# Kernel optimization log

Hardware: AMD Instinct MI355X
Metric: run time of the kernel (lower is better)

The kernel has to match this reference:

```python
import jax, jax.numpy as jnp
import numpy as np

NUM_HEADS = 12
HEAD_SIZE = 64
HIDDEN = NUM_HEADS * HEAD_SIZE  # 768
SEQ = 4096


def setup_inputs() -> dict:
    key = jax.random.key(0)
    ks = jax.random.split(key, 7)
    s = 0.02
    return {
        "hidden_states": jax.random.normal(ks[0], (1, SEQ, HIDDEN), jnp.float32),
        "attention_mask": jnp.zeros((1, 1, 1, SEQ), jnp.float32),
        "Wq": jax.random.normal(ks[1], (HIDDEN, HIDDEN), jnp.float32) * s,
        "bq": jax.random.normal(ks[2], (HIDDEN,), jnp.float32) * s,
        "Wk": jax.random.normal(ks[3], (HIDDEN, HIDDEN), jnp.float32) * s,
        "bk": jax.random.normal(ks[4], (HIDDEN,), jnp.float32) * s,
        "Wv": jax.random.normal(ks[5], (HIDDEN, HIDDEN), jnp.float32) * s,
        "bv": jax.random.normal(ks[6], (HIDDEN,), jnp.float32) * s,
    }


def _split_heads(x):
    # [B, S, H] -> [B, nh, S, hd]
    B, S, _ = x.shape
    return x.reshape(B, S, NUM_HEADS, HEAD_SIZE).transpose(0, 2, 1, 3)


def reference(hidden_states, attention_mask, Wq, bq, Wk, bk, Wv, bv):
    # torch Linear: y = x @ W.T + b
    q = _split_heads(hidden_states @ Wq.T + bq)  # [B, nh, S, hd]
    k = _split_heads(hidden_states @ Wk.T + bk)
    scores = jnp.einsum("bhqd,bhkd->bhqk", q, k) / jnp.sqrt(
        jnp.asarray(HEAD_SIZE, hidden_states.dtype)
    )
    scores = scores + attention_mask  # broadcast [1,1,1,S]
    probs = jax.nn.softmax(scores, axis=-1)  # [B, nh, S, S]
    # multi_rand_attn_cuda is a Monte-Carlo approximation of the exact
    # aggregation: probs @ (hidden @ Wv.T + bv), per head. The reference
    # computes the exact expected value (deterministic equivalent).
    v = _split_heads(hidden_states @ Wv.T + bv)  # [B, nh, S, hd]
    ctx = jnp.einsum("bhqk,bhkd->bhqd", probs, v)  # [B, nh, S, hd]
    B, _, S, _ = ctx.shape
    ctx = ctx.transpose(0, 2, 1, 3).reshape(B, S, HIDDEN)
    return ctx
```

## Files before the change

kernel.cpp:

```cpp
#include <hip/hip_runtime.h>
#include <hip/hip_bf16.h>

#define SEQ 4096
#define HID 768
#define NHEAD 12
#define HDIM 64
#define KVB 64
#define NT (SEQ / KVB)
#define PBK 64
#define PNT (HID / PBK)

typedef __attribute__((ext_vector_type(8))) short bf16x8;
typedef __attribute__((ext_vector_type(4))) float f32x4;
typedef __attribute__((ext_vector_type(4))) short s16x4;

static __device__ __forceinline__ short f2bf(float f) {
    unsigned u = __builtin_bit_cast(unsigned, f);
    unsigned r = (u + 0x7fffu + ((u >> 16) & 1u)) >> 16;
    return (short)r;
}
static __device__ __forceinline__ float bf2f(unsigned short u) {
    return __builtin_bit_cast(float, (unsigned)u << 16);
}
static __device__ __forceinline__ unsigned cvtpk(float lo, float hi) {
    unsigned r;
    asm("v_cvt_pk_bf16_f32 %0, %1, %2" : "=v"(r) : "v"(lo), "v"(hi));
    return r;
}
static __device__ __forceinline__ float max3f(float a, float b, float c) {
    float r;
    asm("v_max3_f32 %0, %1, %2, %3" : "=v"(r) : "v"(a), "v"(b), "v"(c));
    return r;
}
static __device__ __forceinline__ void glds16(const void* g, void* l) {
    __builtin_amdgcn_global_load_lds(
        (const __attribute__((address_space(1))) unsigned*)g,
        (__attribute__((address_space(3))) unsigned*)l, 16, 0, 0);
}

__global__ __launch_bounds__(256) void cast_bf16_kernel(
    const float* __restrict__ src, short* __restrict__ dst)
{
    const size_t i = (size_t)blockIdx.x * 256 + threadIdx.x;
    const float4* s = reinterpret_cast<const float4*>(src) + i * 2;
    const float4 a = s[0], b = s[1];
    bf16x8 o;
    o[0] = f2bf(a.x); o[1] = f2bf(a.y); o[2] = f2bf(a.z); o[3] = f2bf(a.w);
    o[4] = f2bf(b.x); o[5] = f2bf(b.y); o[6] = f2bf(b.z); o[7] = f2bf(b.w);
    reinterpret_cast<bf16x8*>(dst)[i] = o;
}

__global__ __launch_bounds__(256) void cast_w_kernel(
    const float* __restrict__ Wq, const float* __restrict__ Wk,
    const float* __restrict__ Wv, short* __restrict__ dst)
{
    const int z = blockIdx.y;
    const float* src = (z == 0) ? Wq : ((z == 1) ? Wk : Wv);
    const size_t i = (size_t)blockIdx.x * 256 + threadIdx.x;
    const float4* s = reinterpret_cast<const float4*>(src) + i * 2;
    const float4 a = s[0], b = s[1];
    bf16x8 o;
    o[0] = f2bf(a.x); o[1] = f2bf(a.y); o[2] = f2bf(a.z); o[3] = f2bf(a.w);
    o[4] = f2bf(b.x); o[5] = f2bf(b.y); o[6] = f2bf(b.z); o[7] = f2bf(b.w);
    reinterpret_cast<bf16x8*>(dst + (size_t)z * HID * HID)[i] = o;
}

__global__ __launch_bounds__(256) void qkv_proj_kernel(
    const short* __restrict__ hsb, const short* __restrict__ Wb,
    const float* __restrict__ bq, const float* __restrict__ bk,
    const float* __restrict__ bv,
    short* __restrict__ Qb, short* __restrict__ Kb, short* __restrict__ Vt)
{
    __shared__ __align__(16) char lds[65536];
    const int z = blockIdx.z;
    const float* bias = (z == 0) ? bq : ((z == 1) ? bk : bv);

    const int lane = threadIdx.x & 63;
    const int w    = threadIdx.x >> 6;
    const int lr = lane & 15, hi = lane >> 4;
    const int wi = w >> 1, wj = w & 1;

    const short* Ag; const short* Bg; int ar0, br0;
    if (z < 2) { Ag = Wb + (size_t)z * HID * HID; ar0 = blockIdx.x * 128;
                 Bg = hsb;                        br0 = blockIdx.y * 128; }
    else       { Ag = hsb;                        ar0 = blockIdx.y * 128;
                 Bg = Wb + (size_t)2 * HID * HID; br0 = blockIdx.x * 128; }

    const int rsub = lane >> 3;
    const int c16  = (lane & 7) ^ rsub;

    auto stage = [&](int t, int buf) {
        const int k0 = t * PBK;
#pragma unroll
        for (int c = 0; c < 4; ++c) {
            const int ch = w * 4 + c;
            const int row = ch * 8 + rsub;
            glds16(Ag + (size_t)(ar0 + row) * HID + k0 + c16 * 8,
                   lds + buf * 16384 + ch * 1024);
            glds16(Bg + (size_t)(br0 + row) * HID + k0 + c16 * 8,
                   lds + 32768 + buf * 16384 + ch * 1024);
        }
    };

    stage(0, 0);
    f32x4 acc[4][4] = {};

    for (int t = 0; t < PNT; ++t) {
        asm volatile("s_waitcnt vmcnt(0)" ::: "memory");
        __builtin_amdgcn_s_barrier();
        __builtin_amdgcn_sched_barrier(0);
        if (t + 1 < PNT) stage(t + 1, (t + 1) & 1);
        const char* LA = lds + (t & 1) * 16384;
        const char* LB = lds + 32768 + (t & 1) * 16384;
#pragma unroll
        for (int ks = 0; ks < 2; ++ks) {
            bf16x8 af[4], bf_[4];
#pragma unroll
            for (int i = 0; i < 4; ++i) {
                const int rowA = wi * 64 + i * 16 + lr;
                af[i] = *reinterpret_cast<const bf16x8*>(
                    LA + rowA * 128 + (((ks * 4 + hi) ^ (rowA & 7)) << 4));
                const int rowB = wj * 64 + i * 16 + lr;
                bf_[i] = *reinterpret_cast<const bf16x8*>(
                    LB + rowB * 128 + (((ks * 4 + hi) ^ (rowB & 7)) << 4));
            }
            __builtin_amdgcn_s_setprio(1);
#pragma unroll
            for (int ia = 0; ia < 4; ++ia)
#pragma unroll
                for (int ib = 0; ib < 4; ++ib)
                    acc[ia][ib] = __builtin_amdgcn_mfma_f32_16x16x32_bf16(
                        af[ia], bf_[ib], acc[ia][ib], 0, 0, 0);
            __builtin_amdgcn_s_setprio(0);
        }
    }

    const float SCQ = 0.125f * 1.44269504088896340736f;
    if (z < 2) {
        short* outp = (z == 0) ? Qb : Kb;
        const float sc = (z == 0) ? SCQ : 1.0f;
#pragma unroll
        for (int ia = 0; ia < 4; ++ia) {
            const int nb = ar0 + wi * 64 + ia * 16 + hi * 4;
            const float4 b4 = *reinterpret_cast<const float4*>(bias + nb);
#pragma unroll
            for (int ib = 0; ib < 4; ++ib) {
                const int m = br0 + wj * 64 + ib * 16 + lr;
                s16x4 v;
                v[0] = f2bf((acc[ia][ib][0] + b4.x) * sc);
                v[1] = f2bf((acc[ia][ib][1] + b4.y) * sc);
                v[2] = f2bf((acc[ia][ib][2] + b4.z) * sc);
                v[3] = f2bf((acc[ia][ib][3] + b4.w) * sc);
                *reinterpret_cast<s16x4*>(outp + (size_t)m * HID + nb) = v;
            }
        }
    } else {
#pragma unroll
        for (int ib = 0; ib < 4; ++ib) {
            const int n = br0 + wj * 64 + ib * 16 + lr;
            const float bb = bias[n];
#pragma unroll
            for (int ia = 0; ia < 4; ++ia) {
                const int mb = ar0 + wi * 64 + ia * 16 + hi * 4;
                s16x4 v;
                v[0] = f2bf(acc[ia][ib][0] + bb);
                v[1] = f2bf(acc[ia][ib][1] + bb);
                v[2] = f2bf(acc[ia][ib][2] + bb);
                v[3] = f2bf(acc[ia][ib][3] + bb);
                *reinterpret_cast<s16x4*>(Vt + (size_t)n * SEQ + mb) = v;
            }
        }
    }
}

__global__ __launch_bounds__(256, 4) void attn_kernel(
    const short* __restrict__ Qb, const short* __restrict__ Kb,
    const short* __restrict__ Vt, const float* __restrict__ maskp,
    float* __restrict__ out)
{
    __shared__ __align__(16) char lds[40960];
    const int tid  = threadIdx.x;
    const int lane = tid & 63;
    const int w    = tid >> 6;
    const int lr = lane & 15, hi = lane >> 4;
    const int h  = blockIdx.y;
    const int q0 = blockIdx.x * 64 + w * 16;
    const float ML = 1.44269504088896340736f;

    const int srow = lane >> 3;
    auto stage = [&](int t, int buf) {
        const int kt = t * KVB;
#pragma unroll
        for (int j = 0; j < 2; ++j) {
            const int ch  = w * 2 + j;
            const int row = ch * 8 + srow;
            const int c16 = (lane & 7) ^ srow ^ ((ch & 1) << 2);
            glds16(Kb + (size_t)(kt + row) * HID + h * HDIM + c16 * 8,
                   lds + buf * 8192 + ch * 1024);
            glds16(Vt + (size_t)(h * HDIM + row) * SEQ + kt + c16 * 8,
                   lds + 16384 + buf * 8192 + ch * 1024);
        }
    };

    stage(0, 0);

    {
        short* mb = (short*)(lds + 32768);
        const int base = tid * 16;
#pragma unroll
        for (int i = 0; i < 4; ++i) {
            const float4 m4 = *reinterpret_cast<const float4*>(maskp + base + i * 4);
            s16x4 v;
            v[0] = f2bf(m4.x * ML); v[1] = f2bf(m4.y * ML);
            v[2] = f2bf(m4.z * ML); v[3] = f2bf(m4.w * ML);
            *reinterpret_cast<s16x4*>(mb + base + i * 4) = v;
        }
    }

    const short* qp = Qb + (size_t)(q0 + lr) * HID + h * HDIM + hi * 8;
    const bf16x8 qa0 = *reinterpret_cast<const bf16x8*>(qp);
    const bf16x8 qa1 = *reinterpret_cast<const bf16x8*>(qp + 32);

    __syncthreads();

    f32x4 oAcc[4] = {};
    float m_r = -INFINITY, ls = 0.f;
    const short* mlds = (const short*)(lds + 32768);

    const int kbase = ((lr >> 2) * 8) + (lr & 3);
    const int fv    = (lr & 7) ^ ((lr >> 1) & 4);

    for (int t = 0; t < NT; ++t) {
        const int kt = t * KVB;
        asm volatile("s_waitcnt vmcnt(0)" ::: "memory");
        __builtin_amdgcn_s_barrier();
        __builtin_amdgcn_sched_barrier(0);
        if (t + 1 < NT) stage(t + 1, (t + 1) & 1);

        const char* KT = lds + (t & 1) * 8192;
        float s2[4][4];
#pragma unroll
        for (int g = 0; g < 4; ++g) {
            const int mk0 = hi * 8 + (g & 1) * 4 + (g >> 1) * 32;
            const s16x4 mkv = *reinterpret_cast<const s16x4*>(mlds + kt + mk0);
            f32x4 zz;
            zz[0] = bf2f((unsigned short)mkv[0]);
            zz[1] = bf2f((unsigned short)mkv[1]);
            zz[2] = bf2f((unsigned short)mkv[2]);
            zz[3] = bf2f((unsigned short)mkv[3]);
            const int row = kbase + (g & 1) * 4 + (g >> 1) * 32;
            const int fr  = (row & 7) ^ ((row >> 1) & 4);
            const bf16x8 kf0 = *reinterpret_cast<const bf16x8*>(
                KT + row * 128 + ((hi ^ fr) << 4));
            const bf16x8 kf1 = *reinterpret_cast<const bf16x8*>(
                KT + row * 128 + (((4 + hi) ^ fr) << 4));
            __builtin_amdgcn_s_setprio(1);
            zz = __builtin_amdgcn_mfma_f32_16x16x32_bf16(kf0, qa0, zz, 0, 0, 0);
            zz = __builtin_amdgcn_mfma_f32_16x16x32_bf16(kf1, qa1, zz, 0, 0, 0);
            __builtin_amdgcn_s_setprio(0);
            s2[g][0] = zz[0]; s2[g][1] = zz[1]; s2[g][2] = zz[2]; s2[g][3] = zz[3];
        }

        float tmax;
        {
            const float a = max3f(s2[0][0], s2[0][1], s2[0][2]);
            const float b = max3f(s2[0][3], s2[1][0], s2[1][1]);
            const float c = max3f(s2[1][2], s2[1][3], s2[2][0]);
            const float d = max3f(s2[2][1], s2[2][2], s2[2][3]);
            const float e = max3f(s2[3][0], s2[3][1], s2[3][2]);
            tmax = max3f(max3f(a, b, c), max3f(d, e, s2[3][3]),
                         __builtin_bit_cast(float, 0xff800000u));
        }
        tmax = fmaxf(tmax, __shfl_xor(tmax, 16));
        tmax = fmaxf(tmax, __shfl_xor(tmax, 32));

        if (__ballot(tmax > m_r + 8.f)) {
            const float newm = fmaxf(m_r, tmax);
            const float sc = exp2f(fmaxf(m_r - newm, -128.f));
            ls *= sc;
#pragma unroll
            for (int c = 0; c < 4; ++c) oAcc[c] *= sc;
            m_r = newm;
        }

        float e_[4][4];
#pragma unroll
        for (int g = 0; g < 4; ++g) {
#pragma unroll
            for (int r = 0; r < 4; ++r) {
                e_[g][r] = exp2f(s2[g][r] - m_r);
                ls += e_[g][r];
            }
        }
        union { unsigned u[4]; bf16x8 v; } P0, P1;
        P0.u[0] = cvtpk(e_[0][0], e_[0][1]); P0.u[1] = cvtpk(e_[0][2], e_[0][3]);
        P0.u[2] = cvtpk(e_[1][0], e_[1][1]); P0.u[3] = cvtpk(e_[1][2], e_[1][3]);
        P1.u[0] = cvtpk(e_[2][0], e_[2][1]); P1.u[1] = cvtpk(e_[2][2], e_[2][3]);
        P1.u[2] = cvtpk(e_[3][0], e_[3][1]); P1.u[3] = cvtpk(e_[3][2], e_[3][3]);

        const char* VT = lds + 16384 + (t & 1) * 8192;
#pragma unroll
        for (int dg = 0; dg < 4; ++dg) {
            const int rb = (dg * 16 + lr) * 128;
            const bf16x8 v0 = *reinterpret_cast<const bf16x8*>(VT + rb + ((hi ^ fv) << 4));
            const bf16x8 v1 = *reinterpret_cast<const bf16x8*>(VT + rb + (((4 + hi) ^ fv) << 4));
            __builtin_amdgcn_s_setprio(1);
            oAcc[dg] = __builtin_amdgcn_mfma_f32_16x16x32_bf16(v0, P0.v, oAcc[dg], 0, 0, 0);
            oAcc[dg] = __builtin_amdgcn_mfma_f32_16x16x32_bf16(v1, P1.v, oAcc[dg], 0, 0, 0);
            __builtin_amdgcn_s_setprio(0);
        }
    }

    float lt = ls;
    lt += __shfl_xor(lt, 16);
    lt += __shfl_xor(lt, 32);
    const float rl = 1.0f / lt;
    float* ob = out + (size_t)(q0 + lr) * HID + h * HDIM + hi * 4;
#pragma unroll
    for (int dg = 0; dg < 4; ++dg)
        *reinterpret_cast<f32x4*>(ob + dg * 16) = oAcc[dg] * rl;
}

extern "C" void kernel_launch(void* const* d_in, const int* in_sizes, int n_in,
                              void* d_out, int out_size, void* d_ws, size_t ws_size,
                              hipStream_t stream) {
    const float* hs   = (const float*)d_in[0];
    const float* mask = (const float*)d_in[1];
    const float* Wq   = (const float*)d_in[2];
    const float* bq   = (const float*)d_in[3];
    const float* Wk   = (const float*)d_in[4];
    const float* bk   = (const float*)d_in[5];
    const float* Wv   = (const float*)d_in[6];
    const float* bv   = (const float*)d_in[7];

    short* Qb = (short*)d_ws;
    short* Kb = Qb + (size_t)SEQ * HID;
    short* Vt = Kb + (size_t)SEQ * HID;
    float* out = (float*)d_out;

    short* hsb = (short*)d_out;
    short* Wb  = hsb + (size_t)SEQ * HID;

    cast_bf16_kernel<<<dim3(SEQ * HID / 2048), 256, 0, stream>>>(hs, hsb);
    cast_w_kernel<<<dim3(HID * HID / 2048, 3), 256, 0, stream>>>(Wq, Wk, Wv, Wb);

    qkv_proj_kernel<<<dim3(HID / 128, SEQ / 128, 3), 256, 0, stream>>>(
        hsb, Wb, bq, bk, bv, Qb, Kb, Vt);

    attn_kernel<<<dim3(SEQ / KVB, NHEAD), 256, 0, stream>>>(Qb, Kb, Vt, mask, out);
}
```

Before: 151.9 us.

## Split KV tile across wave pairs, each wave handling 32 queries with merge

Each block's four waves are reorganised into two query halves times two key halves. Every wave now processes 32 queries against half of each 64-key tile, so each K and V fragment read from LDS feeds two MFMAs. The two key halves are merged at the end through LDS using max/sum rescaling. The mask is kept as fp32 in LDS and loaded straight in as the MFMA accumulator init instead of being converted from bf16. The cost is more registers and LDS per block, with occupancy lowered to 3, plus an extra merge phase with two block barriers.

```diff
diff --git a/kernel.cpp b/kernel.cpp
--- a/kernel.cpp
+++ b/kernel.cpp
@@ -18,9 +18,6 @@
     unsigned u = __builtin_bit_cast(unsigned, f);
     unsigned r = (u + 0x7fffu + ((u >> 16) & 1u)) >> 16;
     return (short)r;
-}
-static __device__ __forceinline__ float bf2f(unsigned short u) {
-    return __builtin_bit_cast(float, (unsigned)u << 16);
 }
 static __device__ __forceinline__ unsigned cvtpk(float lo, float hi) {
     unsigned r;
@@ -173,18 +170,19 @@
     }
 }
 
-__global__ __launch_bounds__(256, 4) void attn_kernel(
+__global__ __launch_bounds__(256, 3) void attn_kernel(
     const short* __restrict__ Qb, const short* __restrict__ Kb,
     const short* __restrict__ Vt, const float* __restrict__ maskp,
     float* __restrict__ out)
 {
-    __shared__ __align__(16) char lds[40960];
+    __shared__ __align__(16) char lds[49152];
     const int tid  = threadIdx.x;
     const int lane = tid & 63;
     const int w    = tid >> 6;
     const int lr = lane & 15, hi = lane >> 4;
+    const int qh = w >> 1, kh = w & 1;
     const int h  = blockIdx.y;
-    const int q0 = blockIdx.x * 64 + w * 16;
+    const int q0 = blockIdx.x * 64 + qh * 32;
     const float ML = 1.44269504088896340736f;
 
     const int srow = lane >> 3;
@@ -205,120 +203,164 @@
     stage(0, 0);
 
     {
-        short* mb = (short*)(lds + 32768);
+        float* mb = (float*)(lds + 32768);
         const int base = tid * 16;
 #pragma unroll
         for (int i = 0; i < 4; ++i) {
-            const float4 m4 = *reinterpret_cast<const float4*>(maskp + base + i * 4);
-            s16x4 v;
-            v[0] = f2bf(m4.x * ML); v[1] = f2bf(m4.y * ML);
-            v[2] = f2bf(m4.z * ML); v[3] = f2bf(m4.w * ML);
-            *reinterpret_cast<s16x4*>(mb + base + i * 4) = v;
-        }
-    }
-
-    const short* qp = Qb + (size_t)(q0 + lr) * HID + h * HDIM + hi * 8;
-    const bf16x8 qa0 = *reinterpret_cast<const bf16x8*>(qp);
-    const bf16x8 qa1 = *reinterpret_cast<const bf16x8*>(qp + 32);
+            float4 m4 = *reinterpret_cast<const float4*>(maskp + base + i * 4);
+            m4.x *= ML; m4.y *= ML; m4.z *= ML; m4.w *= ML;
+            *reinterpret_cast<float4*>(mb + base + i * 4) = m4;
+        }
+    }
+
+    const short* qbase = Qb + (size_t)(q0 + lr) * HID + h * HDIM + hi * 8;
+    bf16x8 qf[2][2];
+    qf[0][0] = *reinterpret_cast<const bf16x8*>(qbase);
+    qf[0][1] = *reinterpret_cast<const bf16x8*>(qbase + 32);
+    qf[1][0] = *reinterpret_cast<const bf16x8*>(qbase + 16 * HID);
+    qf[1][1] = *reinterpret_cast<const bf16x8*>(qbase + 16 * HID + 32);
 
     __syncthreads();
 
-    f32x4 oAcc[4] = {};
-    float m_r = -INFINITY, ls = 0.f;
-    const short* mlds = (const short*)(lds + 32768);
-
-    const int kbase = ((lr >> 2) * 8) + (lr & 3);
-    const int fv    = (lr & 7) ^ ((lr >> 1) & 4);
+    f32x4 acc[4][2] = {};
+    float m_r[2] = {-INFINITY, -INFINITY};
+    float ls[2]  = {0.f, 0.f};
+    const int kbase = ((lr >> 2) * 8) + (lr & 3) + kh * 32;
+    const int fv    = (lr & 7) ^ (((lr >> 3) & 1) << 2);
+    const int vslot = ((kh * 4 + hi) ^ fv) << 4;
 
     for (int t = 0; t < NT; ++t) {
-        const int kt = t * KVB;
         asm volatile("s_waitcnt vmcnt(0)" ::: "memory");
         __builtin_amdgcn_s_barrier();
         __builtin_amdgcn_sched_barrier(0);
         if (t + 1 < NT) stage(t + 1, (t + 1) & 1);
 
         const char* KT = lds + (t & 1) * 8192;
-        float s2[4][4];
-#pragma unroll
-        for (int g = 0; g < 4; ++g) {
-            const int mk0 = hi * 8 + (g & 1) * 4 + (g >> 1) * 32;
-            const s16x4 mkv = *reinterpret_cast<const s16x4*>(mlds + kt + mk0);
-            f32x4 zz;
-            zz[0] = bf2f((unsigned short)mkv[0]);
-            zz[1] = bf2f((unsigned short)mkv[1]);
-            zz[2] = bf2f((unsigned short)mkv[2]);
-            zz[3] = bf2f((unsigned short)mkv[3]);
-            const int row = kbase + (g & 1) * 4 + (g >> 1) * 32;
+        const float* mk = (const float*)(lds + 32768) + t * KVB + kh * 32 + hi * 8;
+        float s2[2][2][4];
+#pragma unroll
+        for (int kg = 0; kg < 2; ++kg) {
+            const int row = kbase + kg * 4;
             const int fr  = (row & 7) ^ ((row >> 1) & 4);
             const bf16x8 kf0 = *reinterpret_cast<const bf16x8*>(
                 KT + row * 128 + ((hi ^ fr) << 4));
             const bf16x8 kf1 = *reinterpret_cast<const bf16x8*>(
                 KT + row * 128 + (((4 + hi) ^ fr) << 4));
+            const f32x4 ci = *reinterpret_cast<const f32x4*>(mk + kg * 4);
             __builtin_amdgcn_s_setprio(1);
-            zz = __builtin_amdgcn_mfma_f32_16x16x32_bf16(kf0, qa0, zz, 0, 0, 0);
-            zz = __builtin_amdgcn_mfma_f32_16x16x32_bf16(kf1, qa1, zz, 0, 0, 0);
+#pragma unroll
+            for (int qg = 0; qg < 2; ++qg) {
+                f32x4 zz = ci;
+                zz = __builtin_amdgcn_mfma_f32_16x16x32_bf16(kf0, qf[qg][0], zz, 0, 0, 0);
+                zz = __builtin_amdgcn_mfma_f32_16x16x32_bf16(kf1, qf[qg][1], zz, 0, 0, 0);
+                s2[kg][qg][0] = zz[0]; s2[kg][qg][1] = zz[1];
+                s2[kg][qg][2] = zz[2]; s2[kg][qg][3] = zz[3];
+            }
             __builtin_amdgcn_s_setprio(0);
-            s2[g][0] = zz[0]; s2[g][1] = zz[1]; s2[g][2] = zz[2]; s2[g][3] = zz[3];
-        }
-
-        float tmax;
-        {
-            const float a = max3f(s2[0][0], s2[0][1], s2[0][2]);
-            const float b = max3f(s2[0][3], s2[1][0], s2[1][1]);
-            const float c = max3f(s2[1][2], s2[1][3], s2[2][0]);
-            const float d = max3f(s2[2][1], s2[2][2], s2[2][3]);
-            const float e = max3f(s2[3][0], s2[3][1], s2[3][2]);
-            tmax = max3f(max3f(a, b, c), max3f(d, e, s2[3][3]),
-                         __builtin_bit_cast(float, 0xff800000u));
-        }
-        tmax = fmaxf(tmax, __shfl_xor(tmax, 16));
-        tmax = fmaxf(tmax, __shfl_xor(tmax, 32));
-
-        if (__ballot(tmax > m_r + 8.f)) {
-            const float newm = fmaxf(m_r, tmax);
-            const float sc = exp2f(fmaxf(m_r - newm, -128.f));
-            ls *= sc;
-#pragma unroll
-            for (int c = 0; c < 4; ++c) oAcc[c] *= sc;
-            m_r = newm;
-        }
-
-        float e_[4][4];
-#pragma unroll
-        for (int g = 0; g < 4; ++g) {
-#pragma unroll
-            for (int r = 0; r < 4; ++r) {
-                e_[g][r] = exp2f(s2[g][r] - m_r);
-                ls += e_[g][r];
-            }
-        }
-        union { unsigned u[4]; bf16x8 v; } P0, P1;
-        P0.u[0] = cvtpk(e_[0][0], e_[0][1]); P0.u[1] = cvtpk(e_[0][2], e_[0][3]);
-        P0.u[2] = cvtpk(e_[1][0], e_[1][1]); P0.u[3] = cvtpk(e_[1][2], e_[1][3]);
-        P1.u[0] = cvtpk(e_[2][0], e_[2][1]); P1.u[1] = cvtpk(e_[2][2], e_[2][3]);
-        P1.u[2] = cvtpk(e_[3][0], e_[3][1]); P1.u[3] = cvtpk(e_[3][2], e_[3][3]);
+        }
+
+        float tmax[2];
+#pragma unroll
+        for (int qg = 0; qg < 2; ++qg) {
+            const float a = max3f(s2[0][qg][0], s2[0][qg][1], s2[0][qg][2]);
+            const float b = max3f(s2[0][qg][3], s2[1][qg][0], s2[1][qg][1]);
+            const float c = max3f(s2[1][qg][2], s2[1][qg][3], a);
+            float t_ = fmaxf(b, c);
+            t_ = fmaxf(t_, __shfl_xor(t_, 16));
+            t_ = fmaxf(t_, __shfl_xor(t_, 32));
+            tmax[qg] = t_;
+        }
+
+        const bool need = (tmax[0] > m_r[0] + 8.f) || (tmax[1] > m_r[1] + 8.f);
+        if (__ballot(need)) {
+#pragma unroll
+            for (int qg = 0; qg < 2; ++qg) {
+                const float newm = fmaxf(m_r[qg], tmax[qg]);
+                const float sc = exp2f(fmaxf(m_r[qg] - newm, -128.f));
+                ls[qg] *= sc;
+#pragma unroll
+                for (int dg = 0; dg < 4; ++dg) acc[dg][qg] *= sc;
+                m_r[qg] = newm;
+            }
+        }
+
+        union { unsigned u[4]; bf16x8 v; } P[2];
+#pragma unroll
+        for (int qg = 0; qg < 2; ++qg) {
+            float e0 = exp2f(s2[0][qg][0] - m_r[qg]);
+            float e1 = exp2f(s2[0][qg][1] - m_r[qg]);
+            float e2 = exp2f(s2[0][qg][2] - m_r[qg]);
+            float e3 = exp2f(s2[0][qg][3] - m_r[qg]);
+            float e4 = exp2f(s2[1][qg][0] - m_r[qg]);
+            float e5 = exp2f(s2[1][qg][1] - m_r[qg]);
+            float e6 = exp2f(s2[1][qg][2] - m_r[qg]);
+            float e7 = exp2f(s2[1][qg][3] - m_r[qg]);
+            ls[qg] += ((e0 + e1) + (e2 + e3)) + ((e4 + e5) + (e6 + e7));
+            P[qg].u[0] = cvtpk(e0, e1); P[qg].u[1] = cvtpk(e2, e3);
+            P[qg].u[2] = cvtpk(e4, e5); P[qg].u[3] = cvtpk(e6, e7);
+        }
 
         const char* VT = lds + 16384 + (t & 1) * 8192;
 #pragma unroll
         for (int dg = 0; dg < 4; ++dg) {
-            const int rb = (dg * 16 + lr) * 128;
-            const bf16x8 v0 = *reinterpret_cast<const bf16x8*>(VT + rb + ((hi ^ fv) << 4));
-            const bf16x8 v1 = *reinterpret_cast<const bf16x8*>(VT + rb + (((4 + hi) ^ fv) << 4));
+            const bf16x8 vf = *reinterpret_cast<const bf16x8*>(
+                VT + (dg * 16 + lr) * 128 + vslot);
             __builtin_amdgcn_s_setprio(1);
-            oAcc[dg] = __builtin_amdgcn_mfma_f32_16x16x32_bf16(v0, P0.v, oAcc[dg], 0, 0, 0);
-            oAcc[dg] = __builtin_amdgcn_mfma_f32_16x16x32_bf16(v1, P1.v, oAcc[dg], 0, 0, 0);
+            acc[dg][0] = __builtin_amdgcn_mfma_f32_16x16x32_bf16(vf, P[0].v, acc[dg][0], 0, 0, 0);
+            acc[dg][1] = __builtin_amdgcn_mfma_f32_16x16x32_bf16(vf, P[1].v, acc[dg][1], 0, 0, 0);
             __builtin_amdgcn_s_setprio(0);
         }
     }
 
-    float lt = ls;
-    lt += __shfl_xor(lt, 16);
-    lt += __shfl_xor(lt, 32);
-    const float rl = 1.0f / lt;
-    float* ob = out + (size_t)(q0 + lr) * HID + h * HDIM + hi * 4;
-#pragma unroll
-    for (int dg = 0; dg < 4; ++dg)
-        *reinterpret_cast<f32x4*>(ob + dg * 16) = oAcc[dg] * rl;
+#pragma unroll
+    for (int qg = 0; qg < 2; ++qg) {
+        float t_ = ls[qg];
+        t_ += __shfl_xor(t_, 16);
+        t_ += __shfl_xor(t_, 32);
+        ls[qg] = t_;
+    }
+
+    __syncthreads();
+    float* mg = (float*)lds;
+    float* mlb = (float*)(lds + 16384);
+    if (kh == 1) {
+#pragma unroll
+        for (int qg = 0; qg < 2; ++qg) {
+            float2 v; v.x = m_r[qg]; v.y = ls[qg];
+            *reinterpret_cast<float2*>(mlb + (((qh * 2 + qg) * 64 + lane) * 2)) = v;
+        }
+#pragma unroll
+        for (int dg = 0; dg < 4; ++dg)
+#pragma unroll
+            for (int qg = 0; qg < 2; ++qg)
+                *reinterpret_cast<f32x4*>(
+                    mg + ((qh * 8 + dg * 2 + qg) * 64 + lane) * 4) = acc[dg][qg];
+    }
+    __syncthreads();
+    if (kh == 0) {
+        float sc0[2], sc1[2], rl[2];
+#pragma unroll
+        for (int qg = 0; qg < 2; ++qg) {
+            const float2 v = *reinterpret_cast<const float2*>(
+                mlb + (((qh * 2 + qg) * 64 + lane) * 2));
+            const float mm = fmaxf(m_r[qg], v.x);
+            sc0[qg] = exp2f(m_r[qg] - mm);
+            sc1[qg] = exp2f(v.x - mm);
+            rl[qg] = 1.0f / (ls[qg] * sc0[qg] + v.y * sc1[qg]);
+        }
+#pragma unroll
+        for (int dg = 0; dg < 4; ++dg) {
+#pragma unroll
+            for (int qg = 0; qg < 2; ++qg) {
+                const f32x4 o1 = *reinterpret_cast<const f32x4*>(
+                    mg + ((qh * 8 + dg * 2 + qg) * 64 + lane) * 4);
+                const f32x4 of = (acc[dg][qg] * sc0[qg] + o1 * sc1[qg]) * rl[qg];
+                float* op = out + (size_t)(q0 + qg * 16 + lr) * HID
+                          + h * HDIM + dg * 16 + hi * 4;
+                *reinterpret_cast<f32x4*>(op) = of;
+            }
+        }
+    }
 }
 
 extern "C" void kernel_launch(void* const* d_in, const int* in_sizes, int n_in,
```

Result: faster. 148.5 us (-2.2%).

## Split KV tile across wave pairs with LDS merge of partial softmax states

Applied to the files above, without the earlier changes.

The attention kernel now handles 32 queries per block instead of 64. Each pair of waves splits every 64-key tile in half, so each wave computes scores for 32 keys and does one PV MFMA per d-group. The two partial (max, sum, accumulator) states are merged through LDS at the end. The online-softmax rescale check now tests the exponentiated probabilities against a threshold, which skips the per-tile cross-lane max reduction in the common case. The grid doubles, giving more blocks for occupancy, but K/V tiles are loaded twice as often per query and an extra sync and merge epilogue is added.

```diff
diff --git a/kernel.cpp b/kernel.cpp
--- a/kernel.cpp
+++ b/kernel.cpp
@@ -183,8 +183,9 @@
     const int lane = tid & 63;
     const int w    = tid >> 6;
     const int lr = lane & 15, hi = lane >> 4;
+    const int qh = w >> 1, kh = w & 1;
     const int h  = blockIdx.y;
-    const int q0 = blockIdx.x * 64 + w * 16;
+    const int q0 = blockIdx.x * 32 + qh * 16;
     const float ML = 1.44269504088896340736f;
 
     const int srow = lane >> 3;
@@ -207,118 +208,152 @@
     {
         short* mb = (short*)(lds + 32768);
         const int base = tid * 16;
+        float4 m4[4];
+#pragma unroll
+        for (int i = 0; i < 4; ++i)
+            m4[i] = *reinterpret_cast<const float4*>(maskp + base + i * 4);
+        union { unsigned u[8]; } pk;
 #pragma unroll
         for (int i = 0; i < 4; ++i) {
-            const float4 m4 = *reinterpret_cast<const float4*>(maskp + base + i * 4);
-            s16x4 v;
-            v[0] = f2bf(m4.x * ML); v[1] = f2bf(m4.y * ML);
-            v[2] = f2bf(m4.z * ML); v[3] = f2bf(m4.w * ML);
-            *reinterpret_cast<s16x4*>(mb + base + i * 4) = v;
-        }
+            pk.u[i * 2]     = cvtpk(m4[i].x * ML, m4[i].y * ML);
+            pk.u[i * 2 + 1] = cvtpk(m4[i].z * ML, m4[i].w * ML);
+        }
+        *reinterpret_cast<uint4*>(mb + base)     = *reinterpret_cast<uint4*>(&pk.u[0]);
+        *reinterpret_cast<uint4*>(mb + base + 8) = *reinterpret_cast<uint4*>(&pk.u[4]);
     }
 
     const short* qp = Qb + (size_t)(q0 + lr) * HID + h * HDIM + hi * 8;
-    const bf16x8 qa0 = *reinterpret_cast<const bf16x8*>(qp);
-    const bf16x8 qa1 = *reinterpret_cast<const bf16x8*>(qp + 32);
+    const bf16x8 qf0 = *reinterpret_cast<const bf16x8*>(qp);
+    const bf16x8 qf1 = *reinterpret_cast<const bf16x8*>(qp + 32);
 
     __syncthreads();
 
-    f32x4 oAcc[4] = {};
+    f32x4 acc[4] = {};
     float m_r = -INFINITY, ls = 0.f;
+    const int kbase = ((lr >> 2) * 8) + (lr & 3) + kh * 32;
+    const int fv    = (lr & 7) ^ (((lr >> 3) & 1) << 2);
+    const int vslot = ((kh * 4 + hi) ^ fv) << 4;
     const short* mlds = (const short*)(lds + 32768);
 
-    const int kbase = ((lr >> 2) * 8) + (lr & 3);
-    const int fv    = (lr & 7) ^ ((lr >> 1) & 4);
-
     for (int t = 0; t < NT; ++t) {
-        const int kt = t * KVB;
         asm volatile("s_waitcnt vmcnt(0)" ::: "memory");
         __builtin_amdgcn_s_barrier();
         __builtin_amdgcn_sched_barrier(0);
         if (t + 1 < NT) stage(t + 1, (t + 1) & 1);
 
+        const bf16x8 mv = *reinterpret_cast<const bf16x8*>(
+            mlds + t * KVB + kh * 32 + hi * 8);
+        f32x4 ci0, ci1;
+#pragma unroll
+        for (int r = 0; r < 4; ++r) {
+            ci0[r] = bf2f((unsigned short)mv[r]);
+            ci1[r] = bf2f((unsigned short)mv[4 + r]);
+        }
+
         const char* KT = lds + (t & 1) * 8192;
-        float s2[4][4];
-#pragma unroll
-        for (int g = 0; g < 4; ++g) {
-            const int mk0 = hi * 8 + (g & 1) * 4 + (g >> 1) * 32;
-            const s16x4 mkv = *reinterpret_cast<const s16x4*>(mlds + kt + mk0);
-            f32x4 zz;
-            zz[0] = bf2f((unsigned short)mkv[0]);
-            zz[1] = bf2f((unsigned short)mkv[1]);
-            zz[2] = bf2f((unsigned short)mkv[2]);
-            zz[3] = bf2f((unsigned short)mkv[3]);
-            const int row = kbase + (g & 1) * 4 + (g >> 1) * 32;
+        float s2[2][4];
+#pragma unroll
+        for (int kg = 0; kg < 2; ++kg) {
+            const int row = kbase + kg * 4;
             const int fr  = (row & 7) ^ ((row >> 1) & 4);
             const bf16x8 kf0 = *reinterpret_cast<const bf16x8*>(
                 KT + row * 128 + ((hi ^ fr) << 4));
             const bf16x8 kf1 = *reinterpret_cast<const bf16x8*>(
                 KT + row * 128 + (((4 + hi) ^ fr) << 4));
+            f32x4 zz = (kg == 0) ? ci0 : ci1;
             __builtin_amdgcn_s_setprio(1);
-            zz = __builtin_amdgcn_mfma_f32_16x16x32_bf16(kf0, qa0, zz, 0, 0, 0);
-            zz = __builtin_amdgcn_mfma_f32_16x16x32_bf16(kf1, qa1, zz, 0, 0, 0);
+            zz = __builtin_amdgcn_mfma_f32_16x16x32_bf16(kf0, qf0, zz, 0, 0, 0);
+            zz = __builtin_amdgcn_mfma_f32_16x16x32_bf16(kf1, qf1, zz, 0, 0, 0);
             __builtin_amdgcn_s_setprio(0);
-            s2[g][0] = zz[0]; s2[g][1] = zz[1]; s2[g][2] = zz[2]; s2[g][3] = zz[3];
-        }
-
-        float tmax;
-        {
-            const float a = max3f(s2[0][0], s2[0][1], s2[0][2]);
-            const float b = max3f(s2[0][3], s2[1][0], s2[1][1]);
-            const float c = max3f(s2[1][2], s2[1][3], s2[2][0]);
-            const float d = max3f(s2[2][1], s2[2][2], s2[2][3]);
-            const float e = max3f(s2[3][0], s2[3][1], s2[3][2]);
-            tmax = max3f(max3f(a, b, c), max3f(d, e, s2[3][3]),
-                         __builtin_bit_cast(float, 0xff800000u));
-        }
-        tmax = fmaxf(tmax, __shfl_xor(tmax, 16));
-        tmax = fmaxf(tmax, __shfl_xor(tmax, 32));
-
-        if (__ballot(tmax > m_r + 8.f)) {
-            const float newm = fmaxf(m_r, tmax);
+            s2[kg][0] = zz[0]; s2[kg][1] = zz[1];
+            s2[kg][2] = zz[2]; s2[kg][3] = zz[3];
+        }
+
+        float e_[2][4];
+#pragma unroll
+        for (int kg = 0; kg < 2; ++kg)
+#pragma unroll
+            for (int r = 0; r < 4; ++r)
+                e_[kg][r] = exp2f(s2[kg][r] - m_r);
+
+        const float pa = max3f(e_[0][0], e_[0][1], e_[0][2]);
+        const float pb = max3f(e_[0][3], e_[1][0], e_[1][1]);
+        const float pc = max3f(e_[1][2], e_[1][3], pa);
+        const float pmax = fmaxf(pb, pc);
+        if (__ballot(pmax > 256.f)) {
+            float t_ = fmaxf(
+                max3f(s2[0][0], s2[0][1], s2[0][2]),
+                max3f(fmaxf(s2[0][3], s2[1][0]),
+                      fmaxf(s2[1][1], s2[1][2]), s2[1][3]));
+            t_ = fmaxf(t_, __shfl_xor(t_, 16));
+            t_ = fmaxf(t_, __shfl_xor(t_, 32));
+            const float newm = fmaxf(m_r, t_);
             const float sc = exp2f(fmaxf(m_r - newm, -128.f));
             ls *= sc;
 #pragma unroll
-            for (int c = 0; c < 4; ++c) oAcc[c] *= sc;
+            for (int dg = 0; dg < 4; ++dg) acc[dg] *= sc;
             m_r = newm;
-        }
-
-        float e_[4][4];
-#pragma unroll
-        for (int g = 0; g < 4; ++g) {
-#pragma unroll
-            for (int r = 0; r < 4; ++r) {
-                e_[g][r] = exp2f(s2[g][r] - m_r);
-                ls += e_[g][r];
-            }
-        }
-        union { unsigned u[4]; bf16x8 v; } P0, P1;
-        P0.u[0] = cvtpk(e_[0][0], e_[0][1]); P0.u[1] = cvtpk(e_[0][2], e_[0][3]);
-        P0.u[2] = cvtpk(e_[1][0], e_[1][1]); P0.u[3] = cvtpk(e_[1][2], e_[1][3]);
-        P1.u[0] = cvtpk(e_[2][0], e_[2][1]); P1.u[1] = cvtpk(e_[2][2], e_[2][3]);
-        P1.u[2] = cvtpk(e_[3][0], e_[3][1]); P1.u[3] = cvtpk(e_[3][2], e_[3][3]);
+#pragma unroll
+            for (int kg = 0; kg < 2; ++kg)
+#pragma unroll
+                for (int r = 0; r < 4; ++r)
+                    e_[kg][r] = exp2f(s2[kg][r] - newm);
+        }
+
+        ls += ((e_[0][0] + e_[0][1]) + (e_[0][2] + e_[0][3]))
+            + ((e_[1][0] + e_[1][1]) + (e_[1][2] + e_[1][3]));
+        union { unsigned u[4]; bf16x8 v; } P;
+        P.u[0] = cvtpk(e_[0][0], e_[0][1]);
+        P.u[1] = cvtpk(e_[0][2], e_[0][3]);
+        P.u[2] = cvtpk(e_[1][0], e_[1][1]);
+        P.u[3] = cvtpk(e_[1][2], e_[1][3]);
 
         const char* VT = lds + 16384 + (t & 1) * 8192;
 #pragma unroll
         for (int dg = 0; dg < 4; ++dg) {
-            const int rb = (dg * 16 + lr) * 128;
-            const bf16x8 v0 = *reinterpret_cast<const bf16x8*>(VT + rb + ((hi ^ fv) << 4));
-            const bf16x8 v1 = *reinterpret_cast<const bf16x8*>(VT + rb + (((4 + hi) ^ fv) << 4));
+            const bf16x8 vf = *reinterpret_cast<const bf16x8*>(
+                VT + (dg * 16 + lr) * 128 + vslot);
             __builtin_amdgcn_s_setprio(1);
-            oAcc[dg] = __builtin_amdgcn_mfma_f32_16x16x32_bf16(v0, P0.v, oAcc[dg], 0, 0, 0);
-            oAcc[dg] = __builtin_amdgcn_mfma_f32_16x16x32_bf16(v1, P1.v, oAcc[dg], 0, 0, 0);
+            acc[dg] = __builtin_amdgcn_mfma_f32_16x16x32_bf16(vf, P.v, acc[dg], 0, 0, 0);
             __builtin_amdgcn_s_setprio(0);
         }
     }
 
-    float lt = ls;
-    lt += __shfl_xor(lt, 16);
-    lt += __shfl_xor(lt, 32);
-    const float rl = 1.0f / lt;
-    float* ob = out + (size_t)(q0 + lr) * HID + h * HDIM + hi * 4;
-#pragma unroll
-    for (int dg = 0; dg < 4; ++dg)
-        *reinterpret_cast<f32x4*>(ob + dg * 16) = oAcc[dg] * rl;
+    {
+        float t_ = ls;
+        t_ += __shfl_xor(t_, 16);
+        t_ += __shfl_xor(t_, 32);
+        ls = t_;
+    }
+
+    __syncthreads();
+    float* mg  = (float*)lds;
+    float* mlb = (float*)(lds + 8192);
+    if (kh == 1) {
+        float2 v0; v0.x = m_r; v0.y = ls;
+        *reinterpret_cast<float2*>(mlb + (qh * 64 + lane) * 2) = v0;
+#pragma unroll
+        for (int dg = 0; dg < 4; ++dg)
+            *reinterpret_cast<f32x4*>(
+                mg + ((qh * 4 + dg) * 64 + lane) * 4) = acc[dg];
+    }
+    __syncthreads();
+    if (kh == 0) {
+        const float2 v = *reinterpret_cast<const float2*>(
+            mlb + (qh * 64 + lane) * 2);
+        const float mm = fmaxf(m_r, v.x);
+        const float sc0 = exp2f(fmaxf(m_r - mm, -128.f));
+        const float sc1 = exp2f(fmaxf(v.x - mm, -128.f));
+        const float rl = 1.0f / (ls * sc0 + v.y * sc1);
+#pragma unroll
+        for (int dg = 0; dg < 4; ++dg) {
+            const f32x4 o1 = *reinterpret_cast<const f32x4*>(
+                mg + ((qh * 4 + dg) * 64 + lane) * 4);
+            const f32x4 of = (acc[dg] * sc0 + o1 * sc1) * rl;
+            float* op = out + (size_t)(q0 + lr) * HID + h * HDIM + dg * 16 + hi * 4;
+            *reinterpret_cast<f32x4*>(op) = of;
+        }
+    }
 }
 
 extern "C" void kernel_launch(void* const* d_in, const int* in_sizes, int n_in,
@@ -347,5 +382,5 @@
     qkv_proj_kernel<<<dim3(HID / 128, SEQ / 128, 3), 256, 0, stream>>>(
         hsb, Wb, bq, bk, bv, Qb, Kb, Vt);
 
-    attn_kernel<<<dim3(SEQ / KVB, NHEAD), 256, 0, stream>>>(Qb, Kb, Vt, mask, out);
-}
+    attn_kernel<<<dim3(SEQ / 32, NHEAD), 256, 0, stream>>>(Qb, Kb, Vt, mask, out);
+}
```

Result: no change. 151.9 us (+0.0%).

## Use 32x32 MFMA with split-K waves and lazy power-of-two rescaling in attention

Applied to the files above, without the earlier changes.

Reorganizes the attention kernel so each wave handles 32 queries over half of each 64-key tile using 32x32x16 bf16 MFMAs. The two key-halves are merged at the end through LDS with a log-sum-exp combine. The online softmax now exponentiates first and rescales by a power of two only when probabilities exceed 256, which removes the per-tile max reduction and shuffles. It also keeps the mask in fp32, precomputes staging addresses and unrolls by two tiles. The cost is more LDS and a lower occupancy bound (3 blocks instead of 4), plus an extra merge phase at the end.

```diff
diff --git a/kernel.cpp b/kernel.cpp
--- a/kernel.cpp
+++ b/kernel.cpp
@@ -1,5 +1,6 @@
 #include <hip/hip_runtime.h>
 #include <hip/hip_bf16.h>
+#include <math.h>
 
 #define SEQ 4096
 #define HID 768
@@ -12,15 +13,13 @@
 
 typedef __attribute__((ext_vector_type(8))) short bf16x8;
 typedef __attribute__((ext_vector_type(4))) float f32x4;
+typedef __attribute__((ext_vector_type(16))) float f32x16;
 typedef __attribute__((ext_vector_type(4))) short s16x4;
 
 static __device__ __forceinline__ short f2bf(float f) {
     unsigned u = __builtin_bit_cast(unsigned, f);
     unsigned r = (u + 0x7fffu + ((u >> 16) & 1u)) >> 16;
     return (short)r;
-}
-static __device__ __forceinline__ float bf2f(unsigned short u) {
-    return __builtin_bit_cast(float, (unsigned)u << 16);
 }
 static __device__ __forceinline__ unsigned cvtpk(float lo, float hi) {
     unsigned r;
@@ -173,152 +172,206 @@
     }
 }
 
-__global__ __launch_bounds__(256, 4) void attn_kernel(
+__global__ __launch_bounds__(256, 3) void attn_kernel(
     const short* __restrict__ Qb, const short* __restrict__ Kb,
     const short* __restrict__ Vt, const float* __restrict__ maskp,
     float* __restrict__ out)
 {
-    __shared__ __align__(16) char lds[40960];
+    __shared__ __align__(16) char lds[49152];
     const int tid  = threadIdx.x;
     const int lane = tid & 63;
     const int w    = tid >> 6;
-    const int lr = lane & 15, hi = lane >> 4;
-    const int h  = blockIdx.y;
-    const int q0 = blockIdx.x * 64 + w * 16;
+    const int qh = w >> 1, kh = w & 1;
+    const int hl = lane >> 5, q = lane & 31;
+    const int head = blockIdx.y;
+    const int q0w  = blockIdx.x * 64 + qh * 32;
     const float ML = 1.44269504088896340736f;
 
     const int srow = lane >> 3;
-    auto stage = [&](int t, int buf) {
-        const int kt = t * KVB;
-#pragma unroll
-        for (int j = 0; j < 2; ++j) {
-            const int ch  = w * 2 + j;
-            const int row = ch * 8 + srow;
-            const int c16 = (lane & 7) ^ srow ^ ((ch & 1) << 2);
-            glds16(Kb + (size_t)(kt + row) * HID + h * HDIM + c16 * 8,
-                   lds + buf * 8192 + ch * 1024);
-            glds16(Vt + (size_t)(h * HDIM + row) * SEQ + kt + c16 * 8,
-                   lds + 16384 + buf * 8192 + ch * 1024);
-        }
+    int sofK[2], sofV[2];
+    char* sdK[2][2]; char* sdV[2][2];
+#pragma unroll
+    for (int j = 0; j < 2; ++j) {
+        const int ch  = w * 2 + j;
+        const int row = ch * 8 + srow;
+        const int c16 = (lane & 7) ^ srow ^ ((ch & 1) << 2);
+        sofK[j] = row * HID + c16 * 8;
+        sofV[j] = row * SEQ + c16 * 8;
+#pragma unroll
+        for (int b = 0; b < 2; ++b) {
+            sdK[b][j] = lds + b * 8192 + ch * 1024;
+            sdV[b][j] = lds + 16384 + b * 8192 + ch * 1024;
+        }
+    }
+    const short* gK = Kb + head * HDIM;
+    const short* gV = Vt + (size_t)head * HDIM * SEQ;
+    auto stagep = [&](int buf) {
+        glds16(gK + sofK[0], sdK[buf][0]);
+        glds16(gK + sofK[1], sdK[buf][1]);
+        glds16(gV + sofV[0], sdV[buf][0]);
+        glds16(gV + sofV[1], sdV[buf][1]);
+        gK += KVB * HID; gV += KVB;
     };
 
-    stage(0, 0);
+    stagep(0);
 
     {
-        short* mb = (short*)(lds + 32768);
+        float* mb = (float*)(lds + 32768);
         const int base = tid * 16;
 #pragma unroll
         for (int i = 0; i < 4; ++i) {
-            const float4 m4 = *reinterpret_cast<const float4*>(maskp + base + i * 4);
-            s16x4 v;
-            v[0] = f2bf(m4.x * ML); v[1] = f2bf(m4.y * ML);
-            v[2] = f2bf(m4.z * ML); v[3] = f2bf(m4.w * ML);
-            *reinterpret_cast<s16x4*>(mb + base + i * 4) = v;
-        }
-    }
-
-    const short* qp = Qb + (size_t)(q0 + lr) * HID + h * HDIM + hi * 8;
-    const bf16x8 qa0 = *reinterpret_cast<const bf16x8*>(qp);
-    const bf16x8 qa1 = *reinterpret_cast<const bf16x8*>(qp + 32);
+            float4 m4 = *reinterpret_cast<const float4*>(maskp + base + i * 4);
+            m4.x *= ML; m4.y *= ML; m4.z *= ML; m4.w *= ML;
+            *reinterpret_cast<float4*>(mb + base + i * 4) = m4;
+        }
+    }
+
+    const short* qp = Qb + (size_t)(q0w + q) * HID + head * HDIM + hl * 8;
+    const bf16x8 qv0 = *reinterpret_cast<const bf16x8*>(qp);
+    const bf16x8 qv1 = *reinterpret_cast<const bf16x8*>(qp + 16);
+    const bf16x8 qv2 = *reinterpret_cast<const bf16x8*>(qp + 32);
+    const bf16x8 qv3 = *reinterpret_cast<const bf16x8*>(qp + 48);
 
     __syncthreads();
 
-    f32x4 oAcc[4] = {};
-    float m_r = -INFINITY, ls = 0.f;
-    const short* mlds = (const short*)(lds + 32768);
-
-    const int kbase = ((lr >> 2) * 8) + (lr & 3);
-    const int fv    = (lr & 7) ^ ((lr >> 1) & 4);
-
-    for (int t = 0; t < NT; ++t) {
-        const int kt = t * KVB;
+    const int pr = (q & 3) + ((q >> 2) & 1) * 8 + ((q >> 3) & 1) * 4
+                 + ((q >> 4) & 1) * 16;
+    const int krow = kh * 32 + pr;
+    const int fr   = (krow & 7) ^ ((krow >> 1) & 4);
+    const char* kp[2][4];
+    const char* vp[2][2][2];
+#pragma unroll
+    for (int b = 0; b < 2; ++b) {
+#pragma unroll
+        for (int s = 0; s < 4; ++s)
+            kp[b][s] = lds + b * 8192 + krow * 128 + (((s * 2 + hl) ^ fr) << 4);
+#pragma unroll
+        for (int dgrp = 0; dgrp < 2; ++dgrp) {
+            const int vr  = dgrp * 32 + q;
+            const int fvr = (vr & 7) ^ ((vr >> 1) & 4);
+#pragma unroll
+            for (int ksl = 0; ksl < 2; ++ksl)
+                vp[b][dgrp][ksl] = lds + 16384 + b * 8192 + vr * 128
+                                 + (((kh * 4 + ksl * 2 + hl) ^ fvr) << 4);
+        }
+    }
+
+    f32x16 acc0 = {}, acc1 = {};
+    float m_r = 0.f, ls = 0.f;
+
+    auto tile = [&](int tt, int buf) {
         asm volatile("s_waitcnt vmcnt(0)" ::: "memory");
         __builtin_amdgcn_s_barrier();
         __builtin_amdgcn_sched_barrier(0);
-        if (t + 1 < NT) stage(t + 1, (t + 1) & 1);
-
-        const char* KT = lds + (t & 1) * 8192;
-        float s2[4][4];
-#pragma unroll
-        for (int g = 0; g < 4; ++g) {
-            const int mk0 = hi * 8 + (g & 1) * 4 + (g >> 1) * 32;
-            const s16x4 mkv = *reinterpret_cast<const s16x4*>(mlds + kt + mk0);
-            f32x4 zz;
-            zz[0] = bf2f((unsigned short)mkv[0]);
-            zz[1] = bf2f((unsigned short)mkv[1]);
-            zz[2] = bf2f((unsigned short)mkv[2]);
-            zz[3] = bf2f((unsigned short)mkv[3]);
-            const int row = kbase + (g & 1) * 4 + (g >> 1) * 32;
-            const int fr  = (row & 7) ^ ((row >> 1) & 4);
-            const bf16x8 kf0 = *reinterpret_cast<const bf16x8*>(
-                KT + row * 128 + ((hi ^ fr) << 4));
-            const bf16x8 kf1 = *reinterpret_cast<const bf16x8*>(
-                KT + row * 128 + (((4 + hi) ^ fr) << 4));
-            __builtin_amdgcn_s_setprio(1);
-            zz = __builtin_amdgcn_mfma_f32_16x16x32_bf16(kf0, qa0, zz, 0, 0, 0);
-            zz = __builtin_amdgcn_mfma_f32_16x16x32_bf16(kf1, qa1, zz, 0, 0, 0);
-            __builtin_amdgcn_s_setprio(0);
-            s2[g][0] = zz[0]; s2[g][1] = zz[1]; s2[g][2] = zz[2]; s2[g][3] = zz[3];
-        }
-
-        float tmax;
-        {
-            const float a = max3f(s2[0][0], s2[0][1], s2[0][2]);
-            const float b = max3f(s2[0][3], s2[1][0], s2[1][1]);
-            const float c = max3f(s2[1][2], s2[1][3], s2[2][0]);
-            const float d = max3f(s2[2][1], s2[2][2], s2[2][3]);
-            const float e = max3f(s2[3][0], s2[3][1], s2[3][2]);
-            tmax = max3f(max3f(a, b, c), max3f(d, e, s2[3][3]),
-                         __builtin_bit_cast(float, 0xff800000u));
-        }
-        tmax = fmaxf(tmax, __shfl_xor(tmax, 16));
-        tmax = fmaxf(tmax, __shfl_xor(tmax, 32));
-
-        if (__ballot(tmax > m_r + 8.f)) {
-            const float newm = fmaxf(m_r, tmax);
-            const float sc = exp2f(fmaxf(m_r - newm, -128.f));
-            ls *= sc;
-#pragma unroll
-            for (int c = 0; c < 4; ++c) oAcc[c] *= sc;
-            m_r = newm;
-        }
-
-        float e_[4][4];
-#pragma unroll
-        for (int g = 0; g < 4; ++g) {
-#pragma unroll
-            for (int r = 0; r < 4; ++r) {
-                e_[g][r] = exp2f(s2[g][r] - m_r);
-                ls += e_[g][r];
-            }
-        }
+        if (tt + 1 < NT) stagep(buf ^ 1);
+
+        const float* mk = (const float*)(lds + 32768) + tt * KVB + kh * 32 + hl * 8;
+        const f32x4 c0 = *reinterpret_cast<const f32x4*>(mk);
+        const f32x4 c1 = *reinterpret_cast<const f32x4*>(mk + 4);
+        const f32x4 c2 = *reinterpret_cast<const f32x4*>(mk + 16);
+        const f32x4 c3 = *reinterpret_cast<const f32x4*>(mk + 20);
+        f32x16 z;
+#pragma unroll
+        for (int r = 0; r < 4; ++r) {
+            z[r] = c0[r]; z[4 + r] = c1[r]; z[8 + r] = c2[r]; z[12 + r] = c3[r];
+        }
+
+        const bf16x8 k0 = *reinterpret_cast<const bf16x8*>(kp[buf][0]);
+        const bf16x8 k1 = *reinterpret_cast<const bf16x8*>(kp[buf][1]);
+        const bf16x8 k2 = *reinterpret_cast<const bf16x8*>(kp[buf][2]);
+        const bf16x8 k3 = *reinterpret_cast<const bf16x8*>(kp[buf][3]);
+        __builtin_amdgcn_s_setprio(1);
+        z = __builtin_amdgcn_mfma_f32_32x32x16_bf16(k0, qv0, z, 0, 0, 0);
+        z = __builtin_amdgcn_mfma_f32_32x32x16_bf16(k1, qv1, z, 0, 0, 0);
+        z = __builtin_amdgcn_mfma_f32_32x32x16_bf16(k2, qv2, z, 0, 0, 0);
+        z = __builtin_amdgcn_mfma_f32_32x32x16_bf16(k3, qv3, z, 0, 0, 0);
+        __builtin_amdgcn_s_setprio(0);
+
+        float e[16];
+#pragma unroll
+        for (int r = 0; r < 16; ++r) e[r] = exp2f(z[r] - m_r);
+
+        const float pa = max3f(e[0], e[1], e[2]);
+        const float pb = max3f(e[3], e[4], e[5]);
+        const float pc = max3f(e[6], e[7], e[8]);
+        const float pd = max3f(e[9], e[10], e[11]);
+        const float pe = max3f(e[12], e[13], e[14]);
+        const float pmax = max3f(max3f(pa, pb, pc), max3f(pd, pe, e[15]),
+                                 0.0f);
+        if (__ballot(pmax > 256.f)) {
+            const float pm = fmaxf(pmax, __shfl_xor(pmax, 32));
+            int ex = ilogbf(pm) + 1;
+            if (ex < 0) ex = 0;
+            const float dsc = exp2f((float)-ex);
+            m_r += (float)ex;
+            ls *= dsc;
+            acc0 *= dsc; acc1 *= dsc;
+#pragma unroll
+            for (int r = 0; r < 16; ++r) e[r] *= dsc;
+        }
+
+        ls += (((e[0] + e[1]) + (e[2] + e[3])) + ((e[4] + e[5]) + (e[6] + e[7])))
+            + (((e[8] + e[9]) + (e[10] + e[11])) + ((e[12] + e[13]) + (e[14] + e[15])));
         union { unsigned u[4]; bf16x8 v; } P0, P1;
-        P0.u[0] = cvtpk(e_[0][0], e_[0][1]); P0.u[1] = cvtpk(e_[0][2], e_[0][3]);
-        P0.u[2] = cvtpk(e_[1][0], e_[1][1]); P0.u[3] = cvtpk(e_[1][2], e_[1][3]);
-        P1.u[0] = cvtpk(e_[2][0], e_[2][1]); P1.u[1] = cvtpk(e_[2][2], e_[2][3]);
-        P1.u[2] = cvtpk(e_[3][0], e_[3][1]); P1.u[3] = cvtpk(e_[3][2], e_[3][3]);
-
-        const char* VT = lds + 16384 + (t & 1) * 8192;
-#pragma unroll
-        for (int dg = 0; dg < 4; ++dg) {
-            const int rb = (dg * 16 + lr) * 128;
-            const bf16x8 v0 = *reinterpret_cast<const bf16x8*>(VT + rb + ((hi ^ fv) << 4));
-            const bf16x8 v1 = *reinterpret_cast<const bf16x8*>(VT + rb + (((4 + hi) ^ fv) << 4));
-            __builtin_amdgcn_s_setprio(1);
-            oAcc[dg] = __builtin_amdgcn_mfma_f32_16x16x32_bf16(v0, P0.v, oAcc[dg], 0, 0, 0);
-            oAcc[dg] = __builtin_amdgcn_mfma_f32_16x16x32_bf16(v1, P1.v, oAcc[dg], 0, 0, 0);
-            __builtin_amdgcn_s_setprio(0);
-        }
-    }
-
-    float lt = ls;
-    lt += __shfl_xor(lt, 16);
-    lt += __shfl_xor(lt, 32);
-    const float rl = 1.0f / lt;
-    float* ob = out + (size_t)(q0 + lr) * HID + h * HDIM + hi * 4;
-#pragma unroll
-    for (int dg = 0; dg < 4; ++dg)
-        *reinterpret_cast<f32x4*>(ob + dg * 16) = oAcc[dg] * rl;
+#pragma unroll
+        for (int j = 0; j < 4; ++j) {
+            P0.u[j] = cvtpk(e[2 * j], e[2 * j + 1]);
+            P1.u[j] = cvtpk(e[8 + 2 * j], e[9 + 2 * j]);
+        }
+
+        const bf16x8 v00 = *reinterpret_cast<const bf16x8*>(vp[buf][0][0]);
+        const bf16x8 v01 = *reinterpret_cast<const bf16x8*>(vp[buf][0][1]);
+        const bf16x8 v10 = *reinterpret_cast<const bf16x8*>(vp[buf][1][0]);
+        const bf16x8 v11 = *reinterpret_cast<const bf16x8*>(vp[buf][1][1]);
+        __builtin_amdgcn_s_setprio(1);
+        acc0 = __builtin_amdgcn_mfma_f32_32x32x16_bf16(v00, P0.v, acc0, 0, 0, 0);
+        acc0 = __builtin_amdgcn_mfma_f32_32x32x16_bf16(v01, P1.v, acc0, 0, 0, 0);
+        acc1 = __builtin_amdgcn_mfma_f32_32x32x16_bf16(v10, P0.v, acc1, 0, 0, 0);
+        acc1 = __builtin_amdgcn_mfma_f32_32x32x16_bf16(v11, P1.v, acc1, 0, 0, 0);
+        __builtin_amdgcn_s_setprio(0);
+    };
+
+    for (int t = 0; t < NT; t += 2) {
+        tile(t, 0);
+        tile(t + 1, 1);
+    }
+
+    ls += __shfl_xor(ls, 32);
+
+    __syncthreads();
+    float* mg  = (float*)lds;
+    float* mlb = (float*)(lds + 16384);
+    if (kh) {
+        float2 st; st.x = m_r; st.y = ls;
+        *reinterpret_cast<float2*>(mlb + (qh * 64 + lane) * 2) = st;
+        *reinterpret_cast<f32x16*>(mg + ((qh * 2 + 0) * 64 + lane) * 16) = acc0;
+        *reinterpret_cast<f32x16*>(mg + ((qh * 2 + 1) * 64 + lane) * 16) = acc1;
+    }
+    __syncthreads();
+    if (!kh) {
+        const float2 o1 = *reinterpret_cast<const float2*>(
+            mlb + (qh * 64 + lane) * 2);
+        const float mw = fmaxf(m_r, o1.x);
+        const float s0 = exp2f(m_r - mw);
+        const float s1 = exp2f(o1.x - mw);
+        const float rl = 1.0f / (ls * s0 + o1.y * s1);
+        const f32x16 a1 = *reinterpret_cast<const f32x16*>(
+            mg + ((qh * 2 + 0) * 64 + lane) * 16);
+        const f32x16 b1 = *reinterpret_cast<const f32x16*>(
+            mg + ((qh * 2 + 1) * 64 + lane) * 16);
+        const f32x16 o0 = (acc0 * s0 + a1 * s1) * rl;
+        const f32x16 o2 = (acc1 * s0 + b1 * s1) * rl;
+        float* op = out + (size_t)(q0w + q) * HID + head * HDIM;
+#pragma unroll
+        for (int rq = 0; rq < 4; ++rq) {
+            f32x4 v0, v1;
+#pragma unroll
+            for (int j = 0; j < 4; ++j) { v0[j] = o0[rq * 4 + j]; v1[j] = o2[rq * 4 + j]; }
+            const int d0 = rq * 8 + hl * 4;
+            *reinterpret_cast<f32x4*>(op + d0)      = v0;
+            *reinterpret_cast<f32x4*>(op + 32 + d0) = v1;
+        }
+    }
 }
 
 extern "C" void kernel_launch(void* const* d_in, const int* in_sizes, int n_in,
```

Result: faster. 134.0 us (-11.8%).
